# Kernel tuning notes

Measured on AMD Instinct MI355X. Metric: run time of the kernel, lower is better.

The kernel has to match this reference:

```python
import jax, jax.numpy as jnp
import numpy as np

B, T, E, H, L, V = 2, 1024, 768, 12, 4, 50257
HD = E // H
EPS = 1e-3  # keras LayerNormalization default epsilon


def _ln(x, g, b):
    mu = jnp.mean(x, axis=-1, keepdims=True)
    var = jnp.mean(jnp.square(x - mu), axis=-1, keepdims=True)
    return (x - mu) * jax.lax.rsqrt(var + EPS) * g + b


def setup_inputs() -> dict:
    key = jax.random.key(0)
    ks = jax.random.split(key, 12)
    s = 0.02
    return {
        "tokens": jax.random.randint(ks[0], (B, T), 0, V, dtype=jnp.int64),
        "tok_emb": jax.random.normal(ks[1], (V, E), jnp.float32) * s,
        "pos_emb": jax.random.normal(ks[2], (T, E), jnp.float32) * s,
        "wq": jax.random.normal(ks[3], (L, E, E), jnp.float32) * s,
        "wk": jax.random.normal(ks[4], (L, E, E), jnp.float32) * s,
        "wv": jax.random.normal(ks[5], (L, E, E), jnp.float32) * s,
        "wo": jax.random.normal(ks[6], (L, E, E), jnp.float32) * s,
        "wo_b": jnp.zeros((L, E), jnp.float32),
        "ln1_g": jnp.ones((L, E), jnp.float32),
        "ln1_b": jnp.zeros((L, E), jnp.float32),
        "ln2_g": jnp.ones((L, E), jnp.float32),
        "ln2_b": jnp.zeros((L, E), jnp.float32),
        "ff1_w": jax.random.normal(ks[7], (L, E, 4 * E), jnp.float32) * s,
        "ff1_b": jnp.zeros((L, 4 * E), jnp.float32),
        "ff2_w": jax.random.normal(ks[8], (L, 4 * E, E), jnp.float32) * s,
        "ff2_b": jnp.zeros((L, E), jnp.float32),
        "lnf_g": jnp.ones((E,), jnp.float32),
        "lnf_b": jnp.zeros((E,), jnp.float32),
        "head_w": jax.random.normal(ks[9], (E, V), jnp.float32) * s,
        "head_b": jnp.zeros((V,), jnp.float32),
    }


def _forward(tokens, tok_emb, pos_emb, wq, wk, wv, wo, wo_b,
             ln1_g, ln1_b, ln2_g, ln2_b, ff1_w, ff1_b, ff2_w, ff2_b,
             lnf_g, lnf_b, head_w, head_b):
    x = tok_emb[tokens] + pos_emb[None, :, :]  # [B,T,E]
    tril = jnp.tril(jnp.ones((T, T), dtype=bool))
    scale = jnp.asarray(E, x.dtype) ** -0.5  # NOTE: source scales by emb_dim, not head_size
    neg_inf = jnp.asarray(-jnp.inf, x.dtype)
    for l in range(L):
        h = _ln(x, ln1_g[l], ln1_b[l])
        q = (h @ wq[l]).reshape(B, T, H, HD)
        k = (h @ wk[l]).reshape(B, T, H, HD)
        v = (h @ wv[l]).reshape(B, T, H, HD)
        w = jnp.einsum("bihd,bjhd->bhij", q, k) * scale  # [B,H,T,T]
        w = jnp.where(tril, w, neg_inf)
        # source quirk: softmax over the QUERY axis (axis=1 of [B,T,T]) -> axis=2 here
        w = jax.nn.softmax(w, axis=2)
        att = jnp.einsum("bhij,bjhd->bihd", w, v).reshape(B, T, E)
        x = x + att @ wo[l] + wo_b[l]
        h = _ln(x, ln2_g[l], ln2_b[l])
        ff = jax.nn.relu(h @ ff1_w[l] + ff1_b[l]) @ ff2_w[l] + ff2_b[l]
        x = h + ff  # source: residual is post-LN x, not pre-LN
    x = _ln(x, lnf_g, lnf_b)
    return x @ head_w + head_b  # [B,T,V]


def reference(tokens, tok_emb, pos_emb, wq, wk, wv, wo, wo_b,
              ln1_g, ln1_b, ln2_g, ln2_b, ff1_w, ff1_b, ff2_w, ff2_b,
              lnf_g, lnf_b, head_w, head_b):
    return _forward(tokens, tok_emb, pos_emb, wq, wk, wv, wo, wo_b,
                    ln1_g, ln1_b, ln2_g, ln2_b, ff1_w, ff1_b, ff2_w, ff2_b,
                    lnf_g, lnf_b, head_w, head_b)
```

## Files before the change

kernel.cpp:

```cpp
#include <hip/hip_runtime.h>
#include <math.h>

namespace {
constexpr int kB = 2, kT = 1024, kE = 768, kH = 12, kL = 4, kV = 50257;
constexpr int kHD = 64;
constexpr int kM = kB * kT;
constexpr int kFF = 4 * kE;
constexpr float kEPS = 1e-3f;
constexpr float kSCALE = 0.03608439182435161f;
}

typedef __bf16 bf16x8 __attribute__((ext_vector_type(8)));
typedef float f32x4 __attribute__((ext_vector_type(4)));
typedef unsigned short u16;

__device__ __forceinline__ void split_f(float x, unsigned &hb, unsigned &lb) {
  unsigned xb = __float_as_uint(x);
  hb = xb & 0xFFFF0000u;
  lb = __float_as_uint(x - __uint_as_float(hb)) & 0xFFFF0000u;
}
__device__ __forceinline__ unsigned pk(unsigned b0, unsigned b1) {
  return (b0 >> 16) | b1;
}

__global__ __launch_bounds__(256) void embed_kernel(
    const int* __restrict__ tokens, const float* __restrict__ tok_emb,
    const float* __restrict__ pos_emb, float* __restrict__ x) {
  int gid = blockIdx.x * 256 + threadIdx.x;
  int m = gid / (kE / 4);
  int c = gid % (kE / 4);
  int t = m % kT;
  int tok = tokens[m];
  float4 a = ((const float4*)tok_emb)[(size_t)tok * (kE / 4) + c];
  float4 b = ((const float4*)pos_emb)[(size_t)t * (kE / 4) + c];
  ((float4*)x)[gid] = make_float4(a.x + b.x, a.y + b.y, a.z + b.z, a.w + b.w);
}

__global__ __launch_bounds__(256) void ln_kernel(
    const float* __restrict__ x, const float* __restrict__ g,
    const float* __restrict__ bta, float* __restrict__ out) {
  __shared__ float ssum[256], ssq[256];
  int row = blockIdx.x, tid = threadIdx.x;
  const float* xr = x + (size_t)row * kE;
  float v0 = xr[tid], v1 = xr[tid + 256], v2 = xr[tid + 512];
  ssum[tid] = v0 + v1 + v2;
  ssq[tid] = v0 * v0 + v1 * v1 + v2 * v2;
  __syncthreads();
  for (int off = 128; off > 0; off >>= 1) {
    if (tid < off) { ssum[tid] += ssum[tid + off]; ssq[tid] += ssq[tid + off]; }
    __syncthreads();
  }
  float mu = ssum[0] * (1.f / kE);
  float var = ssq[0] * (1.f / kE) - mu * mu;
  float rstd = rsqrtf(var + kEPS);
  float* orow = out + (size_t)row * kE;
  orow[tid]       = (v0 - mu) * rstd * g[tid]       + bta[tid];
  orow[tid + 256] = (v1 - mu) * rstd * g[tid + 256] + bta[tid + 256];
  orow[tid + 512] = (v2 - mu) * rstd * g[tid + 512] + bta[tid + 512];
}

template <int WMF, int RELU>
__global__ __launch_bounds__(256) void gemm_mfma_kernel(
    const float* __restrict__ A, const float* __restrict__ W,
    const float* __restrict__ bias, const float* __restrict__ addsrc,
    float* __restrict__ C, int N, int K) {
  constexpr int BM = WMF * 32;
  __shared__ __align__(16) u16 Ahi[BM][40], Alo[BM][40];
  __shared__ __align__(16) u16 Whi[128][40], Wlo[128][40];
  const int tid = threadIdx.x;
  const int lane = tid & 63;
  const int w = tid >> 6;
  const int wm = (w >> 1) * (WMF * 16);
  const int wn = (w & 1) * 64;
  const int m0 = blockIdx.y * BM, n0 = blockIdx.x * 128;
  const int fr = lane & 15, fg = lane >> 4;

  const int wnl = tid & 127;
  const int wkh = tid >> 7;
  const bool wok = (n0 + wnl) < N;
  constexpr int AF4 = BM / 32;

  f32x4 acc[WMF][4];
#pragma unroll
  for (int i = 0; i < WMF; ++i)
#pragma unroll
    for (int j = 0; j < 4; ++j) acc[i][j] = f32x4{0.f, 0.f, 0.f, 0.f};

  float4 aR[AF4];
  float wR[16];
#pragma unroll
  for (int q = 0; q < AF4; ++q) {
    int el = tid + q * 256;
    int m = el >> 3, kq = el & 7;
    aR[q] = *(const float4*)&A[(size_t)(m0 + m) * K + kq * 4];
  }
  {
    const float* wp = W + (size_t)(wkh * 16) * N + n0 + wnl;
#pragma unroll
    for (int j = 0; j < 16; ++j) wR[j] = wok ? wp[(size_t)j * N] : 0.f;
  }

  for (int k0 = 0; k0 < K; k0 += 32) {
    __syncthreads();
#pragma unroll
    for (int q = 0; q < AF4; ++q) {
      int el = tid + q * 256;
      int m = el >> 3, kq = el & 7;
      unsigned h0, l0, h1, l1, h2, l2, h3, l3;
      split_f(aR[q].x, h0, l0); split_f(aR[q].y, h1, l1);
      split_f(aR[q].z, h2, l2); split_f(aR[q].w, h3, l3);
      *(uint2*)&Ahi[m][kq * 4] = make_uint2(pk(h0, h1), pk(h2, h3));
      *(uint2*)&Alo[m][kq * 4] = make_uint2(pk(l0, l1), pk(l2, l3));
    }
    {
      unsigned hh[16], ll[16];
#pragma unroll
      for (int j = 0; j < 16; ++j) split_f(wR[j], hh[j], ll[j]);
#pragma unroll
      for (int u = 0; u < 2; ++u) {
        *(uint4*)&Whi[wnl][wkh * 16 + u * 8] = make_uint4(
            pk(hh[u * 8 + 0], hh[u * 8 + 1]), pk(hh[u * 8 + 2], hh[u * 8 + 3]),
            pk(hh[u * 8 + 4], hh[u * 8 + 5]), pk(hh[u * 8 + 6], hh[u * 8 + 7]));
        *(uint4*)&Wlo[wnl][wkh * 16 + u * 8] = make_uint4(
            pk(ll[u * 8 + 0], ll[u * 8 + 1]), pk(ll[u * 8 + 2], ll[u * 8 + 3]),
            pk(ll[u * 8 + 4], ll[u * 8 + 5]), pk(ll[u * 8 + 6], ll[u * 8 + 7]));
      }
    }
    __syncthreads();
    if (k0 + 32 < K) {
#pragma unroll
      for (int q = 0; q < AF4; ++q) {
        int el = tid + q * 256;
        int m = el >> 3, kq = el & 7;
        aR[q] = *(const float4*)&A[(size_t)(m0 + m) * K + (k0 + 32) + kq * 4];
      }
      const float* wp = W + (size_t)(k0 + 32 + wkh * 16) * N + n0 + wnl;
#pragma unroll
      for (int j = 0; j < 16; ++j) wR[j] = wok ? wp[(size_t)j * N] : 0.f;
    }
    bf16x8 ah[WMF], al[WMF];
#pragma unroll
    for (int mi = 0; mi < WMF; ++mi) {
      ah[mi] = *(const bf16x8*)&Ahi[wm + mi * 16 + fr][fg * 8];
      al[mi] = *(const bf16x8*)&Alo[wm + mi * 16 + fr][fg * 8];
    }
#pragma unroll
    for (int nj = 0; nj < 4; ++nj) {
      bf16x8 bh = *(const bf16x8*)&Whi[wn + nj * 16 + fr][fg * 8];
      bf16x8 bl = *(const bf16x8*)&Wlo[wn + nj * 16 + fr][fg * 8];
#pragma unroll
      for (int mi = 0; mi < WMF; ++mi) {
        acc[mi][nj] = __builtin_amdgcn_mfma_f32_16x16x32_bf16(ah[mi], bh, acc[mi][nj], 0, 0, 0);
        acc[mi][nj] = __builtin_amdgcn_mfma_f32_16x16x32_bf16(al[mi], bh, acc[mi][nj], 0, 0, 0);
        acc[mi][nj] = __builtin_amdgcn_mfma_f32_16x16x32_bf16(ah[mi], bl, acc[mi][nj], 0, 0, 0);
      }
    }
  }
#pragma unroll
  for (int mi = 0; mi < WMF; ++mi) {
#pragma unroll
    for (int nj = 0; nj < 4; ++nj) {
#pragma unroll
      for (int r = 0; r < 4; ++r) {
        int row = m0 + wm + mi * 16 + fg * 4 + r;
        int col = n0 + wn + nj * 16 + fr;
        if (col < N) {
          float v = acc[mi][nj][r];
          if (bias) v += bias[col];
          if (addsrc) v += addsrc[(size_t)row * N + col];
          if (RELU) v = fmaxf(v, 0.f);
          C[(size_t)row * N + col] = v;
        }
      }
    }
  }
}

__global__ __launch_bounds__(256) void attn_colstats_kernel(
    const float* __restrict__ q, const float* __restrict__ k,
    float* __restrict__ colm, float* __restrict__ coll) {
  __shared__ __align__(16) float ksT[64][68];
  __shared__ __align__(16) float qsT[64][68];
  __shared__ float red[16][64];
  __shared__ float cm[64], cl[64];
  int bh = blockIdx.x, jt = blockIdx.y;
  int b = bh / kH, h = bh % kH;
  int tid = threadIdx.x, tx = tid & 15, ty = tid >> 4;
  int j0 = jt * 64;
  size_t base = (size_t)b * kT * kE + h * kHD;
#pragma unroll
  for (int r = 0; r < 4; ++r) {
    int idx = tid + r * 256;
    int jl = idx >> 4, dq = (idx & 15) * 4;
    float4 kv = *(const float4*)&k[base + (size_t)(j0 + jl) * kE + dq];
    ksT[dq + 0][jl] = kv.x; ksT[dq + 1][jl] = kv.y;
    ksT[dq + 2][jl] = kv.z; ksT[dq + 3][jl] = kv.w;
  }
  if (tid < 64) { cm[tid] = -INFINITY; cl[tid] = 0.f; }
  __syncthreads();
  for (int it = jt; it < kT / 64; ++it) {
    int i0 = it * 64;
#pragma unroll
    for (int r = 0; r < 4; ++r) {
      int idx = tid + r * 256;
      int il = idx >> 4, dq = (idx & 15) * 4;
      float4 qv = *(const float4*)&q[base + (size_t)(i0 + il) * kE + dq];
      qsT[dq + 0][il] = qv.x; qsT[dq + 1][il] = qv.y;
      qsT[dq + 2][il] = qv.z; qsT[dq + 3][il] = qv.w;
    }
    __syncthreads();
    float s[4][4] = {};
#pragma unroll 8
    for (int d = 0; d < 64; ++d) {
      float4 a4 = *(const float4*)&qsT[d][ty * 4];
      float4 b4 = *(const float4*)&ksT[d][tx * 4];
      float a[4] = {a4.x, a4.y, a4.z, a4.w};
      float bb[4] = {b4.x, b4.y, b4.z, b4.w};
#pragma unroll
      for (int i = 0; i < 4; ++i)
#pragma unroll
        for (int j = 0; j < 4; ++j) s[i][j] += a[i] * bb[j];
    }
    float tmax[4] = {-INFINITY, -INFINITY, -INFINITY, -INFINITY};
#pragma unroll
    for (int i = 0; i < 4; ++i)
#pragma unroll
      for (int j = 0; j < 4; ++j) {
        bool valid = (i0 + ty * 4 + i) >= (j0 + tx * 4 + j);
        s[i][j] = valid ? s[i][j] * kSCALE : -INFINITY;
        tmax[j] = fmaxf(tmax[j], s[i][j]);
      }
#pragma unroll
    for (int j = 0; j < 4; ++j) red[ty][tx * 4 + j] = tmax[j];
    __syncthreads();
    if (tid < 64) {
      float tm = -INFINITY;
#pragma unroll
      for (int r = 0; r < 16; ++r) tm = fmaxf(tm, red[r][tid]);
      float mo = cm[tid], mn = fmaxf(mo, tm);
      cl[tid] *= __expf(mo - mn);
      cm[tid] = mn;
    }
    __syncthreads();
    float ps[4] = {0.f, 0.f, 0.f, 0.f};
#pragma unroll
    for (int j = 0; j < 4; ++j) {
      float mj = cm[tx * 4 + j];
#pragma unroll
      for (int i = 0; i < 4; ++i) ps[j] += __expf(s[i][j] - mj);
    }
#pragma unroll
    for (int j = 0; j < 4; ++j) red[ty][tx * 4 + j] = ps[j];
    __syncthreads();
    if (tid < 64) {
      float a = 0.f;
#pragma unroll
      for (int r = 0; r < 16; ++r) a += red[r][tid];
      cl[tid] += a;
    }
    __syncthreads();
  }
  if (tid < 64) {
    colm[(size_t)bh * kT + j0 + tid] = cm[tid];
    coll[(size_t)bh * kT + j0 + tid] = cl[tid];
  }
}

__global__ __launch_bounds__(256) void attn_av_kernel(
    const float* __restrict__ q, const float* __restrict__ k,
    const float* __restrict__ v, const float* __restrict__ colm,
    const float* __restrict__ coll, float* __restrict__ att) {
  __shared__ __align__(16) float qsT[64][68];
  __shared__ __align__(16) float ksT[64][68];
  __shared__ __align__(16) float Vs[64][64];
  __shared__ float mjs[64], ljs[64];
  float (*Ps)[68] = ksT;
  int bh = blockIdx.x, it = blockIdx.y;
  int b = bh / kH, h = bh % kH;
  int tid = threadIdx.x, tx = tid & 15, ty = tid >> 4;
  int i0 = it * 64;
  size_t base = (size_t)b * kT * kE + h * kHD;
#pragma unroll
  for (int r = 0; r < 4; ++r) {
    int idx = tid + r * 256;
    int il = idx >> 4, dq = (idx & 15) * 4;
    float4 qv = *(const float4*)&q[base + (size_t)(i0 + il) * kE + dq];
    qsT[dq + 0][il] = qv.x; qsT[dq + 1][il] = qv.y;
    qsT[dq + 2][il] = qv.z; qsT[dq + 3][il] = qv.w;
  }
  float acc[4][4] = {};
  for (int jt = 0; jt <= it; ++jt) {
    int j0 = jt * 64;
#pragma unroll
    for (int r = 0; r < 4; ++r) {
      int idx = tid + r * 256;
      int jl = idx >> 4, dq = (idx & 15) * 4;
      float4 kv = *(const float4*)&k[base + (size_t)(j0 + jl) * kE + dq];
      ksT[dq + 0][jl] = kv.x; ksT[dq + 1][jl] = kv.y;
      ksT[dq + 2][jl] = kv.z; ksT[dq + 3][jl] = kv.w;
      *(float4*)&Vs[jl][dq] = *(const float4*)&v[base + (size_t)(j0 + jl) * kE + dq];
    }
    if (tid < 64) {
      mjs[tid] = colm[(size_t)bh * kT + j0 + tid];
      ljs[tid] = 1.f / coll[(size_t)bh * kT + j0 + tid];
    }
    __syncthreads();
    float s[4][4] = {};
#pragma unroll 8
    for (int d = 0; d < 64; ++d) {
      float4 a4 = *(const float4*)&qsT[d][ty * 4];
      float4 b4 = *(const float4*)&ksT[d][tx * 4];
      float a[4] = {a4.x, a4.y, a4.z, a4.w};
      float bb[4] = {b4.x, b4.y, b4.z, b4.w};
#pragma unroll
      for (int i = 0; i < 4; ++i)
#pragma unroll
        for (int j = 0; j < 4; ++j) s[i][j] += a[i] * bb[j];
    }
    __syncthreads();
#pragma unroll
    for (int i = 0; i < 4; ++i)
#pragma unroll
      for (int j = 0; j < 4; ++j) {
        bool valid = (i0 + ty * 4 + i) >= (j0 + tx * 4 + j);
        float p = valid ? __expf(s[i][j] * kSCALE - mjs[tx * 4 + j]) * ljs[tx * 4 + j]
                        : 0.f;
        Ps[tx * 4 + j][ty * 4 + i] = p;
      }
    __syncthreads();
#pragma unroll 8
    for (int j = 0; j < 64; ++j) {
      float4 a4 = *(const float4*)&Ps[j][ty * 4];
      float4 b4 = *(const float4*)&Vs[j][tx * 4];
      float a[4] = {a4.x, a4.y, a4.z, a4.w};
      float bb[4] = {b4.x, b4.y, b4.z, b4.w};
#pragma unroll
      for (int i = 0; i < 4; ++i)
#pragma unroll
        for (int d = 0; d < 4; ++d) acc[i][d] += a[i] * bb[d];
    }
    __syncthreads();
  }
#pragma unroll
  for (int i = 0; i < 4; ++i) {
    size_t off = (size_t)(b * kT + i0 + ty * 4 + i) * kE + h * kHD + tx * 4;
    *(float4*)&att[off] = make_float4(acc[i][0], acc[i][1], acc[i][2], acc[i][3]);
  }
}

extern "C" void kernel_launch(void* const* d_in, const int* in_sizes, int n_in,
                              void* d_out, int out_size, void* d_ws, size_t ws_size,
                              hipStream_t stream) {
  const int* tokens    = (const int*)d_in[0];
  const float* tok_emb = (const float*)d_in[1];
  const float* pos_emb = (const float*)d_in[2];
  const float* wq      = (const float*)d_in[3];
  const float* wk      = (const float*)d_in[4];
  const float* wv      = (const float*)d_in[5];
  const float* wo      = (const float*)d_in[6];
  const float* wo_b    = (const float*)d_in[7];
  const float* ln1_g   = (const float*)d_in[8];
  const float* ln1_b   = (const float*)d_in[9];
  const float* ln2_g   = (const float*)d_in[10];
  const float* ln2_b   = (const float*)d_in[11];
  const float* ff1_w   = (const float*)d_in[12];
  const float* ff1_b   = (const float*)d_in[13];
  const float* ff2_w   = (const float*)d_in[14];
  const float* ff2_b   = (const float*)d_in[15];
  const float* lnf_g   = (const float*)d_in[16];
  const float* lnf_b   = (const float*)d_in[17];
  const float* head_w  = (const float*)d_in[18];
  const float* head_b  = (const float*)d_in[19];
  float* out = (float*)d_out;

  float* ws   = (float*)d_ws;
  float* x    = ws;
  float* hbuf = x    + (size_t)kM * kE;
  float* qb   = hbuf + (size_t)kM * kE;
  float* kb   = qb   + (size_t)kM * kE;
  float* vb   = kb   + (size_t)kM * kE;
  float* attb = vb   + (size_t)kM * kE;
  float* ffb  = attb + (size_t)kM * kE;
  float* cm   = ffb  + (size_t)kM * kFF;
  float* cl   = cm   + (size_t)kB * kH * kT;

  embed_kernel<<<kM * kE / 4 / 256, 256, 0, stream>>>(tokens, tok_emb, pos_emb, x);

  dim3 gQ(kE / 128, kM / 64);
  dim3 gFF1(kFF / 128, kM / 128);
  dim3 gHead((kV + 127) / 128, kM / 128);
  dim3 gAtt(kB * kH, kT / 64);
  for (int l = 0; l < kL; ++l) {
    ln_kernel<<<kM, 256, 0, stream>>>(x, ln1_g + l * kE, ln1_b + l * kE, hbuf);
    gemm_mfma_kernel<2, 0><<<gQ, 256, 0, stream>>>(hbuf, wq + (size_t)l * kE * kE, nullptr, nullptr, qb, kE, kE);
    gemm_mfma_kernel<2, 0><<<gQ, 256, 0, stream>>>(hbuf, wk + (size_t)l * kE * kE, nullptr, nullptr, kb, kE, kE);
    gemm_mfma_kernel<2, 0><<<gQ, 256, 0, stream>>>(hbuf, wv + (size_t)l * kE * kE, nullptr, nullptr, vb, kE, kE);
    attn_colstats_kernel<<<gAtt, 256, 0, stream>>>(qb, kb, cm, cl);
    attn_av_kernel<<<gAtt, 256, 0, stream>>>(qb, kb, vb, cm, cl, attb);
    gemm_mfma_kernel<2, 0><<<gQ, 256, 0, stream>>>(attb, wo + (size_t)l * kE * kE, wo_b + l * kE, x, x, kE, kE);
    ln_kernel<<<kM, 256, 0, stream>>>(x, ln2_g + l * kE, ln2_b + l * kE, hbuf);
    gemm_mfma_kernel<4, 1><<<gFF1, 256, 0, stream>>>(hbuf, ff1_w + (size_t)l * kE * kFF, ff1_b + l * kFF, nullptr, ffb, kFF, kE);
    gemm_mfma_kernel<2, 0><<<gQ, 256, 0, stream>>>(ffb, ff2_w + (size_t)l * kFF * kE, ff2_b + l * kE, hbuf, x, kE, kFF);
  }
  ln_kernel<<<kM, 256, 0, stream>>>(x, lnf_g, lnf_b, hbuf);
  gemm_mfma_kernel<4, 0><<<gHead, 256, 0, stream>>>(hbuf, head_w, head_b, nullptr, out, kV, kE);
}
```

Before: 3.206 ms.

## Pre-split operands to bf16 hi/lo buffers, fuse QKV GEMM, drop head lo-term

Weights are converted once per layer into bf16 hi/lo pairs in a k-blocked transposed layout, and the LayerNorm, attention and FF1 outputs are written directly as hi/lo pairs. The GEMMs then load pre-split data with vector loads instead of re-splitting fp32 in every tile. Q, K and V are computed by one fused GEMM over a concatenated weight, and the head GEMM uses only two MFMA terms (no W lo part). This trades the extra conversion kernels and workspace traffic for cheaper GEMM inner loops, and the head loses some precision.

Result: slower. 4.432 ms (+38.3%).

```diff
diff --git a/kernel.cpp b/kernel.cpp
--- a/kernel.cpp
+++ b/kernel.cpp
@@ -6,6 +6,8 @@
 constexpr int kHD = 64;
 constexpr int kM = kB * kT;
 constexpr int kFF = 4 * kE;
+constexpr int kQS = 3 * kE;
+constexpr int kVP = 50304;
 constexpr float kEPS = 1e-3f;
 constexpr float kSCALE = 0.03608439182435161f;
 }
@@ -38,7 +40,8 @@
 
 __global__ __launch_bounds__(256) void ln_kernel(
     const float* __restrict__ x, const float* __restrict__ g,
-    const float* __restrict__ bta, float* __restrict__ out) {
+    const float* __restrict__ bta, float* __restrict__ outf,
+    u16* __restrict__ outh, u16* __restrict__ outl) {
   __shared__ float ssum[256], ssq[256];
   int row = blockIdx.x, tid = threadIdx.x;
   const float* xr = x + (size_t)row * kE;
@@ -53,20 +56,66 @@
   float mu = ssum[0] * (1.f / kE);
   float var = ssq[0] * (1.f / kE) - mu * mu;
   float rstd = rsqrtf(var + kEPS);
-  float* orow = out + (size_t)row * kE;
-  orow[tid]       = (v0 - mu) * rstd * g[tid]       + bta[tid];
-  orow[tid + 256] = (v1 - mu) * rstd * g[tid + 256] + bta[tid + 256];
-  orow[tid + 512] = (v2 - mu) * rstd * g[tid + 512] + bta[tid + 512];
-}
-
-template <int WMF, int RELU>
-__global__ __launch_bounds__(256) void gemm_mfma_kernel(
-    const float* __restrict__ A, const float* __restrict__ W,
+  size_t rb = (size_t)row * kE;
+#pragma unroll
+  for (int p = 0; p < 3; ++p) {
+    int c = tid + p * 256;
+    float v = (p == 0) ? v0 : (p == 1) ? v1 : v2;
+    float y = (v - mu) * rstd * g[c] + bta[c];
+    if (outf) outf[rb + c] = y;
+    unsigned hb, lb;
+    split_f(y, hb, lb);
+    outh[rb + c] = (u16)(hb >> 16);
+    outl[rb + c] = (u16)(lb >> 16);
+  }
+}
+
+template <int WRITE_LO>
+__global__ __launch_bounds__(256) void wconv_kernel(
+    const float* __restrict__ src, u16* __restrict__ dh, u16* __restrict__ dl,
+    int Nsrc, int Ndt, int colOff) {
+  __shared__ float T[64][68];
+  int nt = blockIdx.x, kt = blockIdx.y, tid = threadIdx.x;
+  int cb = tid & 15, rb = tid >> 4;
+#pragma unroll
+  for (int p = 0; p < 4; ++p) {
+    int r = p * 16 + rb;
+    const float* srow = src + (size_t)(kt * 64 + r) * Nsrc;
+#pragma unroll
+    for (int j = 0; j < 4; ++j) {
+      int n = nt * 64 + cb * 4 + j;
+      T[r][cb * 4 + j] = (n < Nsrc) ? srow[n] : 0.f;
+    }
+  }
+  __syncthreads();
+#pragma unroll
+  for (int q = 0; q < 2; ++q) {
+    int c = tid + q * 256;
+    int gg = c >> 6, n = c & 63;
+    unsigned hh[8], ll[8];
+#pragma unroll
+    for (int j = 0; j < 8; ++j) split_f(T[gg * 8 + j][n], hh[j], ll[j]);
+    size_t o = ((size_t)(kt * 8 + gg) * Ndt + (colOff + nt * 64 + n)) * 8;
+    *(uint4*)&dh[o] = make_uint4(pk(hh[0], hh[1]), pk(hh[2], hh[3]),
+                                 pk(hh[4], hh[5]), pk(hh[6], hh[7]));
+    if (WRITE_LO)
+      *(uint4*)&dl[o] = make_uint4(pk(ll[0], ll[1]), pk(ll[2], ll[3]),
+                                   pk(ll[4], ll[5]), pk(ll[6], ll[7]));
+  }
+}
+
+template <int WMF, int TERMS, int RELU, int OSPLIT>
+__global__ __launch_bounds__(256) void gemm_bf16s_kernel(
+    const u16* __restrict__ Ah, const u16* __restrict__ Al,
+    const u16* __restrict__ Wh, const u16* __restrict__ Wl,
     const float* __restrict__ bias, const float* __restrict__ addsrc,
-    float* __restrict__ C, int N, int K) {
+    float* __restrict__ C, u16* __restrict__ Ch, u16* __restrict__ Cl,
+    int N, int K, int Ndt) {
   constexpr int BM = WMF * 32;
-  __shared__ __align__(16) u16 Ahi[BM][40], Alo[BM][40];
-  __shared__ __align__(16) u16 Whi[128][40], Wlo[128][40];
+  constexpr int AC = WMF / 2;
+  __shared__ __align__(16) u16 Ash[BM][40], Asl[BM][40];
+  __shared__ __align__(16) u16 Wsh[128][40];
+  __shared__ __align__(16) u16 Wsl[TERMS == 3 ? 128 : 1][40];
   const int tid = threadIdx.x;
   const int lane = tid & 63;
   const int w = tid >> 6;
@@ -74,11 +123,8 @@
   const int wn = (w & 1) * 64;
   const int m0 = blockIdx.y * BM, n0 = blockIdx.x * 128;
   const int fr = lane & 15, fg = lane >> 4;
-
-  const int wnl = tid & 127;
-  const int wkh = tid >> 7;
-  const bool wok = (n0 + wnl) < N;
-  constexpr int AF4 = BM / 32;
+  const int wn_l = tid & 127;
+  const int wk8 = (tid >> 7) * 2;
 
   f32x4 acc[WMF][4];
 #pragma unroll
@@ -86,90 +132,87 @@
 #pragma unroll
     for (int j = 0; j < 4; ++j) acc[i][j] = f32x4{0.f, 0.f, 0.f, 0.f};
 
-  float4 aR[AF4];
-  float wR[16];
-#pragma unroll
-  for (int q = 0; q < AF4; ++q) {
-    int el = tid + q * 256;
-    int m = el >> 3, kq = el & 7;
-    aR[q] = *(const float4*)&A[(size_t)(m0 + m) * K + kq * 4];
-  }
-  {
-    const float* wp = W + (size_t)(wkh * 16) * N + n0 + wnl;
-#pragma unroll
-    for (int j = 0; j < 16; ++j) wR[j] = wok ? wp[(size_t)j * N] : 0.f;
-  }
+  uint4 aPh[AC], aPl[AC], wPh[2], wPl[2];
+  (void)wPl;
+
+#define LOAD_TILE(k0_)                                                        \
+  {                                                                           \
+    _Pragma("unroll") for (int q = 0; q < AC; ++q) {                          \
+      int e = tid + q * 256;                                                  \
+      int m = e >> 2, kq = e & 3;                                             \
+      size_t off = (size_t)(m0 + m) * K + (k0_) + kq * 8;                     \
+      aPh[q] = *(const uint4*)&Ah[off];                                       \
+      aPl[q] = *(const uint4*)&Al[off];                                       \
+    }                                                                         \
+    _Pragma("unroll") for (int u = 0; u < 2; ++u) {                           \
+      size_t off = ((size_t)((k0_) / 8 + wk8 + u) * Ndt + (n0 + wn_l)) * 8;   \
+      wPh[u] = *(const uint4*)&Wh[off];                                       \
+      if (TERMS == 3) wPl[u] = *(const uint4*)&Wl[off];                       \
+    }                                                                         \
+  }
+
+  LOAD_TILE(0)
 
   for (int k0 = 0; k0 < K; k0 += 32) {
     __syncthreads();
 #pragma unroll
-    for (int q = 0; q < AF4; ++q) {
-      int el = tid + q * 256;
-      int m = el >> 3, kq = el & 7;
-      unsigned h0, l0, h1, l1, h2, l2, h3, l3;
-      split_f(aR[q].x, h0, l0); split_f(aR[q].y, h1, l1);
-      split_f(aR[q].z, h2, l2); split_f(aR[q].w, h3, l3);
-      *(uint2*)&Ahi[m][kq * 4] = make_uint2(pk(h0, h1), pk(h2, h3));
-      *(uint2*)&Alo[m][kq * 4] = make_uint2(pk(l0, l1), pk(l2, l3));
-    }
-    {
-      unsigned hh[16], ll[16];
-#pragma unroll
-      for (int j = 0; j < 16; ++j) split_f(wR[j], hh[j], ll[j]);
-#pragma unroll
-      for (int u = 0; u < 2; ++u) {
-        *(uint4*)&Whi[wnl][wkh * 16 + u * 8] = make_uint4(
-            pk(hh[u * 8 + 0], hh[u * 8 + 1]), pk(hh[u * 8 + 2], hh[u * 8 + 3]),
-            pk(hh[u * 8 + 4], hh[u * 8 + 5]), pk(hh[u * 8 + 6], hh[u * 8 + 7]));
-        *(uint4*)&Wlo[wnl][wkh * 16 + u * 8] = make_uint4(
-            pk(ll[u * 8 + 0], ll[u * 8 + 1]), pk(ll[u * 8 + 2], ll[u * 8 + 3]),
-            pk(ll[u * 8 + 4], ll[u * 8 + 5]), pk(ll[u * 8 + 6], ll[u * 8 + 7]));
-      }
-    }
-    __syncthreads();
-    if (k0 + 32 < K) {
-#pragma unroll
-      for (int q = 0; q < AF4; ++q) {
-        int el = tid + q * 256;
-        int m = el >> 3, kq = el & 7;
-        aR[q] = *(const float4*)&A[(size_t)(m0 + m) * K + (k0 + 32) + kq * 4];
-      }
-      const float* wp = W + (size_t)(k0 + 32 + wkh * 16) * N + n0 + wnl;
-#pragma unroll
-      for (int j = 0; j < 16; ++j) wR[j] = wok ? wp[(size_t)j * N] : 0.f;
-    }
+    for (int q = 0; q < AC; ++q) {
+      int e = tid + q * 256;
+      int m = e >> 2, kq = e & 3;
+      *(uint4*)&Ash[m][kq * 8] = aPh[q];
+      *(uint4*)&Asl[m][kq * 8] = aPl[q];
+    }
+#pragma unroll
+    for (int u = 0; u < 2; ++u) {
+      *(uint4*)&Wsh[wn_l][(wk8 + u) * 8] = wPh[u];
+      if (TERMS == 3) *(uint4*)&Wsl[wn_l][(wk8 + u) * 8] = wPl[u];
+    }
+    __syncthreads();
+    if (k0 + 32 < K) LOAD_TILE(k0 + 32)
     bf16x8 ah[WMF], al[WMF];
 #pragma unroll
     for (int mi = 0; mi < WMF; ++mi) {
-      ah[mi] = *(const bf16x8*)&Ahi[wm + mi * 16 + fr][fg * 8];
-      al[mi] = *(const bf16x8*)&Alo[wm + mi * 16 + fr][fg * 8];
+      ah[mi] = *(const bf16x8*)&Ash[wm + mi * 16 + fr][fg * 8];
+      al[mi] = *(const bf16x8*)&Asl[wm + mi * 16 + fr][fg * 8];
     }
 #pragma unroll
     for (int nj = 0; nj < 4; ++nj) {
-      bf16x8 bh = *(const bf16x8*)&Whi[wn + nj * 16 + fr][fg * 8];
-      bf16x8 bl = *(const bf16x8*)&Wlo[wn + nj * 16 + fr][fg * 8];
+      bf16x8 bh = *(const bf16x8*)&Wsh[wn + nj * 16 + fr][fg * 8];
 #pragma unroll
       for (int mi = 0; mi < WMF; ++mi) {
         acc[mi][nj] = __builtin_amdgcn_mfma_f32_16x16x32_bf16(ah[mi], bh, acc[mi][nj], 0, 0, 0);
         acc[mi][nj] = __builtin_amdgcn_mfma_f32_16x16x32_bf16(al[mi], bh, acc[mi][nj], 0, 0, 0);
-        acc[mi][nj] = __builtin_amdgcn_mfma_f32_16x16x32_bf16(ah[mi], bl, acc[mi][nj], 0, 0, 0);
       }
-    }
-  }
+      if (TERMS == 3) {
+        bf16x8 bl = *(const bf16x8*)&Wsl[wn + nj * 16 + fr][fg * 8];
+#pragma unroll
+        for (int mi = 0; mi < WMF; ++mi)
+          acc[mi][nj] = __builtin_amdgcn_mfma_f32_16x16x32_bf16(ah[mi], bl, acc[mi][nj], 0, 0, 0);
+      }
+    }
+  }
+#undef LOAD_TILE
 #pragma unroll
   for (int mi = 0; mi < WMF; ++mi) {
 #pragma unroll
     for (int nj = 0; nj < 4; ++nj) {
-#pragma unroll
-      for (int r = 0; r < 4; ++r) {
-        int row = m0 + wm + mi * 16 + fg * 4 + r;
-        int col = n0 + wn + nj * 16 + fr;
-        if (col < N) {
-          float v = acc[mi][nj][r];
-          if (bias) v += bias[col];
-          if (addsrc) v += addsrc[(size_t)row * N + col];
-          if (RELU) v = fmaxf(v, 0.f);
-          C[(size_t)row * N + col] = v;
+      int col = n0 + wn + nj * 16 + fr;
+      if (col < N) {
+#pragma unroll
+        for (int r = 0; r < 4; ++r) {
+          int row = m0 + wm + mi * 16 + fg * 4 + r;
+          float vv = acc[mi][nj][r];
+          if (bias) vv += bias[col];
+          if (addsrc) vv += addsrc[(size_t)row * N + col];
+          if (RELU) vv = fmaxf(vv, 0.f);
+          if (OSPLIT) {
+            unsigned hb, lb;
+            split_f(vv, hb, lb);
+            Ch[(size_t)row * N + col] = (u16)(hb >> 16);
+            Cl[(size_t)row * N + col] = (u16)(lb >> 16);
+          } else {
+            C[(size_t)row * N + col] = vv;
+          }
         }
       }
     }
@@ -187,12 +230,12 @@
   int b = bh / kH, h = bh % kH;
   int tid = threadIdx.x, tx = tid & 15, ty = tid >> 4;
   int j0 = jt * 64;
-  size_t base = (size_t)b * kT * kE + h * kHD;
+  size_t base = (size_t)b * kT * kQS + h * kHD;
 #pragma unroll
   for (int r = 0; r < 4; ++r) {
     int idx = tid + r * 256;
     int jl = idx >> 4, dq = (idx & 15) * 4;
-    float4 kv = *(const float4*)&k[base + (size_t)(j0 + jl) * kE + dq];
+    float4 kv = *(const float4*)&k[base + (size_t)(j0 + jl) * kQS + dq];
     ksT[dq + 0][jl] = kv.x; ksT[dq + 1][jl] = kv.y;
     ksT[dq + 2][jl] = kv.z; ksT[dq + 3][jl] = kv.w;
   }
@@ -204,7 +247,7 @@
     for (int r = 0; r < 4; ++r) {
       int idx = tid + r * 256;
       int il = idx >> 4, dq = (idx & 15) * 4;
-      float4 qv = *(const float4*)&q[base + (size_t)(i0 + il) * kE + dq];
+      float4 qv = *(const float4*)&q[base + (size_t)(i0 + il) * kQS + dq];
       qsT[dq + 0][il] = qv.x; qsT[dq + 1][il] = qv.y;
       qsT[dq + 2][il] = qv.z; qsT[dq + 3][il] = qv.w;
     }
@@ -269,7 +312,8 @@
 __global__ __launch_bounds__(256) void attn_av_kernel(
     const float* __restrict__ q, const float* __restrict__ k,
     const float* __restrict__ v, const float* __restrict__ colm,
-    const float* __restrict__ coll, float* __restrict__ att) {
+    const float* __restrict__ coll, u16* __restrict__ atth,
+    u16* __restrict__ attl) {
   __shared__ __align__(16) float qsT[64][68];
   __shared__ __align__(16) float ksT[64][68];
   __shared__ __align__(16) float Vs[64][64];
@@ -279,12 +323,12 @@
   int b = bh / kH, h = bh % kH;
   int tid = threadIdx.x, tx = tid & 15, ty = tid >> 4;
   int i0 = it * 64;
-  size_t base = (size_t)b * kT * kE + h * kHD;
+  size_t base = (size_t)b * kT * kQS + h * kHD;
 #pragma unroll
   for (int r = 0; r < 4; ++r) {
     int idx = tid + r * 256;
     int il = idx >> 4, dq = (idx & 15) * 4;
-    float4 qv = *(const float4*)&q[base + (size_t)(i0 + il) * kE + dq];
+    float4 qv = *(const float4*)&q[base + (size_t)(i0 + il) * kQS + dq];
     qsT[dq + 0][il] = qv.x; qsT[dq + 1][il] = qv.y;
     qsT[dq + 2][il] = qv.z; qsT[dq + 3][il] = qv.w;
   }
@@ -295,10 +339,10 @@
     for (int r = 0; r < 4; ++r) {
       int idx = tid + r * 256;
       int jl = idx >> 4, dq = (idx & 15) * 4;
-      float4 kv = *(const float4*)&k[base + (size_t)(j0 + jl) * kE + dq];
+      float4 kv = *(const float4*)&k[base + (size_t)(j0 + jl) * kQS + dq];
       ksT[dq + 0][jl] = kv.x; ksT[dq + 1][jl] = kv.y;
       ksT[dq + 2][jl] = kv.z; ksT[dq + 3][jl] = kv.w;
-      *(float4*)&Vs[jl][dq] = *(const float4*)&v[base + (size_t)(j0 + jl) * kE + dq];
+      *(float4*)&Vs[jl][dq] = *(const float4*)&v[base + (size_t)(j0 + jl) * kQS + dq];
     }
     if (tid < 64) {
       mjs[tid] = colm[(size_t)bh * kT + j0 + tid];
@@ -344,7 +388,11 @@
 #pragma unroll
   for (int i = 0; i < 4; ++i) {
     size_t off = (size_t)(b * kT + i0 + ty * 4 + i) * kE + h * kHD + tx * 4;
-    *(float4*)&att[off] = make_float4(acc[i][0], acc[i][1], acc[i][2], acc[i][3]);
+    unsigned h0, l0, h1, l1, h2, l2, h3, l3;
+    split_f(acc[i][0], h0, l0); split_f(acc[i][1], h1, l1);
+    split_f(acc[i][2], h2, l2); split_f(acc[i][3], h3, l3);
+    *(uint2*)&atth[off] = make_uint2(pk(h0, h1), pk(h2, h3));
+    *(uint2*)&attl[off] = make_uint2(pk(l0, l1), pk(l2, l3));
   }
 }
 
@@ -373,35 +421,64 @@
   const float* head_b  = (const float*)d_in[19];
   float* out = (float*)d_out;
 
-  float* ws   = (float*)d_ws;
-  float* x    = ws;
-  float* hbuf = x    + (size_t)kM * kE;
-  float* qb   = hbuf + (size_t)kM * kE;
-  float* kb   = qb   + (size_t)kM * kE;
-  float* vb   = kb   + (size_t)kM * kE;
-  float* attb = vb   + (size_t)kM * kE;
-  float* ffb  = attb + (size_t)kM * kE;
-  float* cm   = ffb  + (size_t)kM * kFF;
-  float* cl   = cm   + (size_t)kB * kH * kT;
+  char* p = (char*)d_ws;
+  float* x    = (float*)p;            p += (size_t)kM * kE * 4;
+  float* hbuf = (float*)p;            p += (size_t)kM * kE * 4;
+  u16* hh     = (u16*)p;              p += (size_t)kM * kE * 2;
+  u16* hl     = (u16*)p;              p += (size_t)kM * kE * 2;
+  float* qkvf = (float*)p;            p += (size_t)kM * kQS * 4;
+  u16* atth   = (u16*)p;              p += (size_t)kM * kE * 2;
+  u16* attl   = (u16*)p;              p += (size_t)kM * kE * 2;
+  u16* ffh    = (u16*)p;              p += (size_t)kM * kFF * 2;
+  u16* ffl    = (u16*)p;              p += (size_t)kM * kFF * 2;
+  float* cm   = (float*)p;            p += (size_t)kB * kH * kT * 4;
+  float* cl   = (float*)p;            p += (size_t)kB * kH * kT * 4;
+  u16* wsw    = (u16*)p;
+  u16* qkvh = wsw;
+  u16* qkvl = qkvh + (size_t)kE * kQS;
+  u16* woh  = qkvl + (size_t)kE * kQS;
+  u16* wol  = woh  + (size_t)kE * kE;
+  u16* f1h  = wol  + (size_t)kE * kE;
+  u16* f1l  = f1h  + (size_t)kE * kFF;
+  u16* f2h  = f1l  + (size_t)kE * kFF;
+  u16* f2l  = f2h  + (size_t)kFF * kE;
+  u16* headH = wsw;
 
   embed_kernel<<<kM * kE / 4 / 256, 256, 0, stream>>>(tokens, tok_emb, pos_emb, x);
 
-  dim3 gQ(kE / 128, kM / 64);
+  dim3 gQKV(kQS / 128, kM / 128);
+  dim3 gE64(kE / 128, kM / 64);
   dim3 gFF1(kFF / 128, kM / 128);
-  dim3 gHead((kV + 127) / 128, kM / 128);
+  dim3 gHead(kVP / 128, kM / 128);
   dim3 gAtt(kB * kH, kT / 64);
+  dim3 cE(kE / 64, kE / 64);
+  dim3 cF1(kFF / 64, kE / 64);
+  dim3 cF2(kE / 64, kFF / 64);
+  dim3 cHd(kVP / 64, kE / 64);
+
   for (int l = 0; l < kL; ++l) {
-    ln_kernel<<<kM, 256, 0, stream>>>(x, ln1_g + l * kE, ln1_b + l * kE, hbuf);
-    gemm_mfma_kernel<2, 0><<<gQ, 256, 0, stream>>>(hbuf, wq + (size_t)l * kE * kE, nullptr, nullptr, qb, kE, kE);
-    gemm_mfma_kernel<2, 0><<<gQ, 256, 0, stream>>>(hbuf, wk + (size_t)l * kE * kE, nullptr, nullptr, kb, kE, kE);
-    gemm_mfma_kernel<2, 0><<<gQ, 256, 0, stream>>>(hbuf, wv + (size_t)l * kE * kE, nullptr, nullptr, vb, kE, kE);
-    attn_colstats_kernel<<<gAtt, 256, 0, stream>>>(qb, kb, cm, cl);
-    attn_av_kernel<<<gAtt, 256, 0, stream>>>(qb, kb, vb, cm, cl, attb);
-    gemm_mfma_kernel<2, 0><<<gQ, 256, 0, stream>>>(attb, wo + (size_t)l * kE * kE, wo_b + l * kE, x, x, kE, kE);
-    ln_kernel<<<kM, 256, 0, stream>>>(x, ln2_g + l * kE, ln2_b + l * kE, hbuf);
-    gemm_mfma_kernel<4, 1><<<gFF1, 256, 0, stream>>>(hbuf, ff1_w + (size_t)l * kE * kFF, ff1_b + l * kFF, nullptr, ffb, kFF, kE);
-    gemm_mfma_kernel<2, 0><<<gQ, 256, 0, stream>>>(ffb, ff2_w + (size_t)l * kFF * kE, ff2_b + l * kE, hbuf, x, kE, kFF);
-  }
-  ln_kernel<<<kM, 256, 0, stream>>>(x, lnf_g, lnf_b, hbuf);
-  gemm_mfma_kernel<4, 0><<<gHead, 256, 0, stream>>>(hbuf, head_w, head_b, nullptr, out, kV, kE);
-}
+    wconv_kernel<1><<<cE, 256, 0, stream>>>(wq + (size_t)l * kE * kE, qkvh, qkvl, kE, kQS, 0);
+    wconv_kernel<1><<<cE, 256, 0, stream>>>(wk + (size_t)l * kE * kE, qkvh, qkvl, kE, kQS, kE);
+    wconv_kernel<1><<<cE, 256, 0, stream>>>(wv + (size_t)l * kE * kE, qkvh, qkvl, kE, kQS, 2 * kE);
+    wconv_kernel<1><<<cE, 256, 0, stream>>>(wo + (size_t)l * kE * kE, woh, wol, kE, kE, 0);
+    wconv_kernel<1><<<cF1, 256, 0, stream>>>(ff1_w + (size_t)l * kE * kFF, f1h, f1l, kFF, kFF, 0);
+    wconv_kernel<1><<<cF2, 256, 0, stream>>>(ff2_w + (size_t)l * kFF * kE, f2h, f2l, kE, kE, 0);
+
+    ln_kernel<<<kM, 256, 0, stream>>>(x, ln1_g + l * kE, ln1_b + l * kE, nullptr, hh, hl);
+    gemm_bf16s_kernel<4, 3, 0, 0><<<gQKV, 256, 0, stream>>>(
+        hh, hl, qkvh, qkvl, nullptr, nullptr, qkvf, nullptr, nullptr, kQS, kE, kQS);
+    attn_colstats_kernel<<<gAtt, 256, 0, stream>>>(qkvf, qkvf + kE, cm, cl);
+    attn_av_kernel<<<gAtt, 256, 0, stream>>>(qkvf, qkvf + kE, qkvf + 2 * kE, cm, cl, atth, attl);
+    gemm_bf16s_kernel<2, 3, 0, 0><<<gE64, 256, 0, stream>>>(
+        atth, attl, woh, wol, wo_b + l * kE, x, x, nullptr, nullptr, kE, kE, kE);
+    ln_kernel<<<kM, 256, 0, stream>>>(x, ln2_g + l * kE, ln2_b + l * kE, hbuf, hh, hl);
+    gemm_bf16s_kernel<4, 3, 1, 1><<<gFF1, 256, 0, stream>>>(
+        hh, hl, f1h, f1l, ff1_b + l * kFF, nullptr, nullptr, ffh, ffl, kFF, kE, kFF);
+    gemm_bf16s_kernel<2, 3, 0, 0><<<gE64, 256, 0, stream>>>(
+        ffh, ffl, f2h, f2l, ff2_b + l * kE, hbuf, x, nullptr, nullptr, kE, kFF, kE);
+  }
+  ln_kernel<<<kM, 256, 0, stream>>>(x, lnf_g, lnf_b, nullptr, hh, hl);
+  wconv_kernel<0><<<cHd, 256, 0, stream>>>(head_w, headH, nullptr, kV, kVP, 0);
+  gemm_bf16s_kernel<4, 2, 0, 0><<<gHead, 256, 0, stream>>>(
+      hh, hl, headH, nullptr, head_b, nullptr, out, nullptr, nullptr, kV, kE, kVP);
+}
```

## Fuse QKV projections into one GEMM and use two-term bf16 split for head

Applied to the files above, without the earlier changes.

Q, K and V projections are computed by a single GEMM launch that selects the weight matrix per column block and writes an interleaved QKV buffer; attention kernels take a row stride. The GEMM kernel gains a TERMS parameter; the vocab head uses only hi*hi and lo*hi bf16 products, dropping the A-hi times W-lo MFMA. Packing of bf16 halves uses a byte-permute builtin. This cuts MFMA work in the largest GEMM and launch overhead, at some accuracy loss in the head output.

After: 2.901 ms. 9.5% less time.

```diff
diff --git a/kernel.cpp b/kernel.cpp
--- a/kernel.cpp
+++ b/kernel.cpp
@@ -6,6 +6,7 @@
 constexpr int kHD = 64;
 constexpr int kM = kB * kT;
 constexpr int kFF = 4 * kE;
+constexpr int kQS = 3 * kE;
 constexpr float kEPS = 1e-3f;
 constexpr float kSCALE = 0.03608439182435161f;
 }
@@ -14,13 +15,15 @@
 typedef float f32x4 __attribute__((ext_vector_type(4)));
 typedef unsigned short u16;
 
-__device__ __forceinline__ void split_f(float x, unsigned &hb, unsigned &lb) {
-  unsigned xb = __float_as_uint(x);
-  hb = xb & 0xFFFF0000u;
-  lb = __float_as_uint(x - __uint_as_float(hb)) & 0xFFFF0000u;
-}
-__device__ __forceinline__ unsigned pk(unsigned b0, unsigned b1) {
-  return (b0 >> 16) | b1;
+__device__ __forceinline__ unsigned pk2hi(float a, float b) {
+#if __has_builtin(__builtin_amdgcn_perm)
+  return __builtin_amdgcn_perm(__float_as_uint(b), __float_as_uint(a), 0x07060302u);
+#else
+  return (__float_as_uint(a) >> 16) | (__float_as_uint(b) & 0xFFFF0000u);
+#endif
+}
+__device__ __forceinline__ float hi_f(float x) {
+  return __uint_as_float(__float_as_uint(x) & 0xFFFF0000u);
 }
 
 __global__ __launch_bounds__(256) void embed_kernel(
@@ -59,9 +62,10 @@
   orow[tid + 512] = (v2 - mu) * rstd * g[tid + 512] + bta[tid + 512];
 }
 
-template <int WMF, int RELU>
+template <int WMF, int TERMS, int RELU>
 __global__ __launch_bounds__(256) void gemm_mfma_kernel(
     const float* __restrict__ A, const float* __restrict__ W,
+    const float* __restrict__ W2, const float* __restrict__ W3, int NW,
     const float* __restrict__ bias, const float* __restrict__ addsrc,
     float* __restrict__ C, int N, int K) {
   constexpr int BM = WMF * 32;
@@ -74,12 +78,22 @@
   const int wn = (w & 1) * 64;
   const int m0 = blockIdx.y * BM, n0 = blockIdx.x * 128;
   const int fr = lane & 15, fg = lane >> 4;
+  if (TERMS == 2 && K < 0) *(volatile u16*)&Wlo[0][0] = 0;
 
   const int wnl = tid & 127;
   const int wkh = tid >> 7;
   const bool wok = (n0 + wnl) < N;
   constexpr int AF4 = BM / 32;
 
+  const float* Wp = W;
+  int ncol = n0;
+  if (W2) {
+    int c = n0 / NW;
+    Wp = (c == 0) ? W : (c == 1) ? W2 : W3;
+    ncol = n0 - c * NW;
+  }
+  const int wstride = W2 ? NW : N;
+
   f32x4 acc[WMF][4];
 #pragma unroll
   for (int i = 0; i < WMF; ++i)
@@ -95,9 +109,9 @@
     aR[q] = *(const float4*)&A[(size_t)(m0 + m) * K + kq * 4];
   }
   {
-    const float* wp = W + (size_t)(wkh * 16) * N + n0 + wnl;
-#pragma unroll
-    for (int j = 0; j < 16; ++j) wR[j] = wok ? wp[(size_t)j * N] : 0.f;
+    const float* wp = Wp + (size_t)(wkh * 16) * wstride + ncol + wnl;
+#pragma unroll
+    for (int j = 0; j < 16; ++j) wR[j] = wok ? wp[(size_t)j * wstride] : 0.f;
   }
 
   for (int k0 = 0; k0 < K; k0 += 32) {
@@ -106,24 +120,31 @@
     for (int q = 0; q < AF4; ++q) {
       int el = tid + q * 256;
       int m = el >> 3, kq = el & 7;
-      unsigned h0, l0, h1, l1, h2, l2, h3, l3;
-      split_f(aR[q].x, h0, l0); split_f(aR[q].y, h1, l1);
-      split_f(aR[q].z, h2, l2); split_f(aR[q].w, h3, l3);
-      *(uint2*)&Ahi[m][kq * 4] = make_uint2(pk(h0, h1), pk(h2, h3));
-      *(uint2*)&Alo[m][kq * 4] = make_uint2(pk(l0, l1), pk(l2, l3));
-    }
-    {
-      unsigned hh[16], ll[16];
-#pragma unroll
-      for (int j = 0; j < 16; ++j) split_f(wR[j], hh[j], ll[j]);
+      float4 av = aR[q];
+      float h0 = hi_f(av.x), h1 = hi_f(av.y), h2 = hi_f(av.z), h3 = hi_f(av.w);
+      *(uint2*)&Ahi[m][kq * 4] = make_uint2(pk2hi(av.x, av.y), pk2hi(av.z, av.w));
+      *(uint2*)&Alo[m][kq * 4] =
+          make_uint2(pk2hi(av.x - h0, av.y - h1), pk2hi(av.z - h2, av.w - h3));
+    }
+    if (TERMS == 3) {
+      float wl[16];
+#pragma unroll
+      for (int j = 0; j < 16; ++j) wl[j] = wR[j] - hi_f(wR[j]);
 #pragma unroll
       for (int u = 0; u < 2; ++u) {
         *(uint4*)&Whi[wnl][wkh * 16 + u * 8] = make_uint4(
-            pk(hh[u * 8 + 0], hh[u * 8 + 1]), pk(hh[u * 8 + 2], hh[u * 8 + 3]),
-            pk(hh[u * 8 + 4], hh[u * 8 + 5]), pk(hh[u * 8 + 6], hh[u * 8 + 7]));
+            pk2hi(wR[u * 8 + 0], wR[u * 8 + 1]), pk2hi(wR[u * 8 + 2], wR[u * 8 + 3]),
+            pk2hi(wR[u * 8 + 4], wR[u * 8 + 5]), pk2hi(wR[u * 8 + 6], wR[u * 8 + 7]));
         *(uint4*)&Wlo[wnl][wkh * 16 + u * 8] = make_uint4(
-            pk(ll[u * 8 + 0], ll[u * 8 + 1]), pk(ll[u * 8 + 2], ll[u * 8 + 3]),
-            pk(ll[u * 8 + 4], ll[u * 8 + 5]), pk(ll[u * 8 + 6], ll[u * 8 + 7]));
+            pk2hi(wl[u * 8 + 0], wl[u * 8 + 1]), pk2hi(wl[u * 8 + 2], wl[u * 8 + 3]),
+            pk2hi(wl[u * 8 + 4], wl[u * 8 + 5]), pk2hi(wl[u * 8 + 6], wl[u * 8 + 7]));
+      }
+    } else {
+#pragma unroll
+      for (int u = 0; u < 2; ++u) {
+        *(uint4*)&Whi[wnl][wkh * 16 + u * 8] = make_uint4(
+            pk2hi(wR[u * 8 + 0], wR[u * 8 + 1]), pk2hi(wR[u * 8 + 2], wR[u * 8 + 3]),
+            pk2hi(wR[u * 8 + 4], wR[u * 8 + 5]), pk2hi(wR[u * 8 + 6], wR[u * 8 + 7]));
       }
     }
     __syncthreads();
@@ -134,9 +155,9 @@
         int m = el >> 3, kq = el & 7;
         aR[q] = *(const float4*)&A[(size_t)(m0 + m) * K + (k0 + 32) + kq * 4];
       }
-      const float* wp = W + (size_t)(k0 + 32 + wkh * 16) * N + n0 + wnl;
-#pragma unroll
-      for (int j = 0; j < 16; ++j) wR[j] = wok ? wp[(size_t)j * N] : 0.f;
+      const float* wp = Wp + (size_t)(k0 + 32 + wkh * 16) * wstride + ncol + wnl;
+#pragma unroll
+      for (int j = 0; j < 16; ++j) wR[j] = wok ? wp[(size_t)j * wstride] : 0.f;
     }
     bf16x8 ah[WMF], al[WMF];
 #pragma unroll
@@ -147,12 +168,16 @@
 #pragma unroll
     for (int nj = 0; nj < 4; ++nj) {
       bf16x8 bh = *(const bf16x8*)&Whi[wn + nj * 16 + fr][fg * 8];
-      bf16x8 bl = *(const bf16x8*)&Wlo[wn + nj * 16 + fr][fg * 8];
 #pragma unroll
       for (int mi = 0; mi < WMF; ++mi) {
         acc[mi][nj] = __builtin_amdgcn_mfma_f32_16x16x32_bf16(ah[mi], bh, acc[mi][nj], 0, 0, 0);
         acc[mi][nj] = __builtin_amdgcn_mfma_f32_16x16x32_bf16(al[mi], bh, acc[mi][nj], 0, 0, 0);
-        acc[mi][nj] = __builtin_amdgcn_mfma_f32_16x16x32_bf16(ah[mi], bl, acc[mi][nj], 0, 0, 0);
+      }
+      if (TERMS == 3) {
+        bf16x8 bl = *(const bf16x8*)&Wlo[wn + nj * 16 + fr][fg * 8];
+#pragma unroll
+        for (int mi = 0; mi < WMF; ++mi)
+          acc[mi][nj] = __builtin_amdgcn_mfma_f32_16x16x32_bf16(ah[mi], bl, acc[mi][nj], 0, 0, 0);
       }
     }
   }
@@ -160,11 +185,11 @@
   for (int mi = 0; mi < WMF; ++mi) {
 #pragma unroll
     for (int nj = 0; nj < 4; ++nj) {
-#pragma unroll
-      for (int r = 0; r < 4; ++r) {
-        int row = m0 + wm + mi * 16 + fg * 4 + r;
-        int col = n0 + wn + nj * 16 + fr;
-        if (col < N) {
+      int col = n0 + wn + nj * 16 + fr;
+      if (col < N) {
+#pragma unroll
+        for (int r = 0; r < 4; ++r) {
+          int row = m0 + wm + mi * 16 + fg * 4 + r;
           float v = acc[mi][nj][r];
           if (bias) v += bias[col];
           if (addsrc) v += addsrc[(size_t)row * N + col];
@@ -178,7 +203,7 @@
 
 __global__ __launch_bounds__(256) void attn_colstats_kernel(
     const float* __restrict__ q, const float* __restrict__ k,
-    float* __restrict__ colm, float* __restrict__ coll) {
+    float* __restrict__ colm, float* __restrict__ coll, int qs) {
   __shared__ __align__(16) float ksT[64][68];
   __shared__ __align__(16) float qsT[64][68];
   __shared__ float red[16][64];
@@ -187,12 +212,12 @@
   int b = bh / kH, h = bh % kH;
   int tid = threadIdx.x, tx = tid & 15, ty = tid >> 4;
   int j0 = jt * 64;
-  size_t base = (size_t)b * kT * kE + h * kHD;
+  size_t base = (size_t)b * kT * qs + h * kHD;
 #pragma unroll
   for (int r = 0; r < 4; ++r) {
     int idx = tid + r * 256;
     int jl = idx >> 4, dq = (idx & 15) * 4;
-    float4 kv = *(const float4*)&k[base + (size_t)(j0 + jl) * kE + dq];
+    float4 kv = *(const float4*)&k[base + (size_t)(j0 + jl) * qs + dq];
     ksT[dq + 0][jl] = kv.x; ksT[dq + 1][jl] = kv.y;
     ksT[dq + 2][jl] = kv.z; ksT[dq + 3][jl] = kv.w;
   }
@@ -204,7 +229,7 @@
     for (int r = 0; r < 4; ++r) {
       int idx = tid + r * 256;
       int il = idx >> 4, dq = (idx & 15) * 4;
-      float4 qv = *(const float4*)&q[base + (size_t)(i0 + il) * kE + dq];
+      float4 qv = *(const float4*)&q[base + (size_t)(i0 + il) * qs + dq];
       qsT[dq + 0][il] = qv.x; qsT[dq + 1][il] = qv.y;
       qsT[dq + 2][il] = qv.z; qsT[dq + 3][il] = qv.w;
     }
@@ -269,7 +294,7 @@
 __global__ __launch_bounds__(256) void attn_av_kernel(
     const float* __restrict__ q, const float* __restrict__ k,
     const float* __restrict__ v, const float* __restrict__ colm,
-    const float* __restrict__ coll, float* __restrict__ att) {
+    const float* __restrict__ coll, float* __restrict__ att, int qs) {
   __shared__ __align__(16) float qsT[64][68];
   __shared__ __align__(16) float ksT[64][68];
   __shared__ __align__(16) float Vs[64][64];
@@ -279,12 +304,12 @@
   int b = bh / kH, h = bh % kH;
   int tid = threadIdx.x, tx = tid & 15, ty = tid >> 4;
   int i0 = it * 64;
-  size_t base = (size_t)b * kT * kE + h * kHD;
+  size_t base = (size_t)b * kT * qs + h * kHD;
 #pragma unroll
   for (int r = 0; r < 4; ++r) {
     int idx = tid + r * 256;
     int il = idx >> 4, dq = (idx & 15) * 4;
-    float4 qv = *(const float4*)&q[base + (size_t)(i0 + il) * kE + dq];
+    float4 qv = *(const float4*)&q[base + (size_t)(i0 + il) * qs + dq];
     qsT[dq + 0][il] = qv.x; qsT[dq + 1][il] = qv.y;
     qsT[dq + 2][il] = qv.z; qsT[dq + 3][il] = qv.w;
   }
@@ -295,10 +320,10 @@
     for (int r = 0; r < 4; ++r) {
       int idx = tid + r * 256;
       int jl = idx >> 4, dq = (idx & 15) * 4;
-      float4 kv = *(const float4*)&k[base + (size_t)(j0 + jl) * kE + dq];
+      float4 kv = *(const float4*)&k[base + (size_t)(j0 + jl) * qs + dq];
       ksT[dq + 0][jl] = kv.x; ksT[dq + 1][jl] = kv.y;
       ksT[dq + 2][jl] = kv.z; ksT[dq + 3][jl] = kv.w;
-      *(float4*)&Vs[jl][dq] = *(const float4*)&v[base + (size_t)(j0 + jl) * kE + dq];
+      *(float4*)&Vs[jl][dq] = *(const float4*)&v[base + (size_t)(j0 + jl) * qs + dq];
     }
     if (tid < 64) {
       mjs[tid] = colm[(size_t)bh * kT + j0 + tid];
@@ -376,32 +401,38 @@
   float* ws   = (float*)d_ws;
   float* x    = ws;
   float* hbuf = x    + (size_t)kM * kE;
-  float* qb   = hbuf + (size_t)kM * kE;
-  float* kb   = qb   + (size_t)kM * kE;
-  float* vb   = kb   + (size_t)kM * kE;
-  float* attb = vb   + (size_t)kM * kE;
+  float* qkvf = hbuf + (size_t)kM * kE;
+  float* attb = qkvf + (size_t)kM * kQS;
   float* ffb  = attb + (size_t)kM * kE;
   float* cm   = ffb  + (size_t)kM * kFF;
   float* cl   = cm   + (size_t)kB * kH * kT;
 
   embed_kernel<<<kM * kE / 4 / 256, 256, 0, stream>>>(tokens, tok_emb, pos_emb, x);
 
-  dim3 gQ(kE / 128, kM / 64);
+  dim3 gQKV(kQS / 128, kM / 128);
+  dim3 gE(kE / 128, kM / 64);
   dim3 gFF1(kFF / 128, kM / 128);
   dim3 gHead((kV + 127) / 128, kM / 128);
   dim3 gAtt(kB * kH, kT / 64);
   for (int l = 0; l < kL; ++l) {
     ln_kernel<<<kM, 256, 0, stream>>>(x, ln1_g + l * kE, ln1_b + l * kE, hbuf);
-    gemm_mfma_kernel<2, 0><<<gQ, 256, 0, stream>>>(hbuf, wq + (size_t)l * kE * kE, nullptr, nullptr, qb, kE, kE);
-    gemm_mfma_kernel<2, 0><<<gQ, 256, 0, stream>>>(hbuf, wk + (size_t)l * kE * kE, nullptr, nullptr, kb, kE, kE);
-    gemm_mfma_kernel<2, 0><<<gQ, 256, 0, stream>>>(hbuf, wv + (size_t)l * kE * kE, nullptr, nullptr, vb, kE, kE);
-    attn_colstats_kernel<<<gAtt, 256, 0, stream>>>(qb, kb, cm, cl);
-    attn_av_kernel<<<gAtt, 256, 0, stream>>>(qb, kb, vb, cm, cl, attb);
-    gemm_mfma_kernel<2, 0><<<gQ, 256, 0, stream>>>(attb, wo + (size_t)l * kE * kE, wo_b + l * kE, x, x, kE, kE);
+    gemm_mfma_kernel<4, 3, 0><<<gQKV, 256, 0, stream>>>(
+        hbuf, wq + (size_t)l * kE * kE, wk + (size_t)l * kE * kE,
+        wv + (size_t)l * kE * kE, kE, nullptr, nullptr, qkvf, kQS, kE);
+    attn_colstats_kernel<<<gAtt, 256, 0, stream>>>(qkvf, qkvf + kE, cm, cl, kQS);
+    attn_av_kernel<<<gAtt, 256, 0, stream>>>(qkvf, qkvf + kE, qkvf + 2 * kE, cm, cl, attb, kQS);
+    gemm_mfma_kernel<2, 3, 0><<<gE, 256, 0, stream>>>(
+        attb, wo + (size_t)l * kE * kE, nullptr, nullptr, 0,
+        wo_b + l * kE, x, x, kE, kE);
     ln_kernel<<<kM, 256, 0, stream>>>(x, ln2_g + l * kE, ln2_b + l * kE, hbuf);
-    gemm_mfma_kernel<4, 1><<<gFF1, 256, 0, stream>>>(hbuf, ff1_w + (size_t)l * kE * kFF, ff1_b + l * kFF, nullptr, ffb, kFF, kE);
-    gemm_mfma_kernel<2, 0><<<gQ, 256, 0, stream>>>(ffb, ff2_w + (size_t)l * kFF * kE, ff2_b + l * kE, hbuf, x, kE, kFF);
+    gemm_mfma_kernel<4, 3, 1><<<gFF1, 256, 0, stream>>>(
+        hbuf, ff1_w + (size_t)l * kE * kFF, nullptr, nullptr, 0,
+        ff1_b + l * kFF, nullptr, ffb, kFF, kE);
+    gemm_mfma_kernel<2, 3, 0><<<gE, 256, 0, stream>>>(
+        ffb, ff2_w + (size_t)l * kFF * kE, nullptr, nullptr, 0,
+        ff2_b + l * kE, hbuf, x, kE, kFF);
   }
   ln_kernel<<<kM, 256, 0, stream>>>(x, lnf_g, lnf_b, hbuf);
-  gemm_mfma_kernel<4, 0><<<gHead, 256, 0, stream>>>(hbuf, head_w, head_b, nullptr, out, kV, kE);
-}
+  gemm_mfma_kernel<4, 2, 0><<<gHead, 256, 0, stream>>>(
+      hbuf, head_w, nullptr, nullptr, 0, head_b, nullptr, out, kV, kE);
+}
```
